# Optimization experiments

Hardware: AMD Instinct MI355X
Metric: run time of the kernel (lower is better)

## Reference

```python
import jax, jax.numpy as jnp
import numpy as np


def setup_inputs() -> dict:
    key = jax.random.key(0)
    k1, k2, k3, k4 = jax.random.split(key, 4)
    B, S, IN, H = 4, 2048, 512, 1024
    x = jax.random.normal(k1, (B, S, IN), dtype=jnp.float32)
    W1 = jax.random.normal(k2, (IN, H), dtype=jnp.float32) * (1.0 / np.sqrt(IN))
    b1 = jax.random.normal(k3, (H,), dtype=jnp.float32) * 0.02
    Wq = jax.random.normal(k4, (H, H), dtype=jnp.float32) * (1.0 / np.sqrt(H))
    return {"x": x, "W1": W1, "b1": b1, "Wq": Wq, "atten_size": 16}


def reference(x, W1, b1, Wq, atten_size):
    A = atten_size
    B, S, _ = x.shape
    H = W1.shape[1]
    h = jax.nn.relu(jnp.einsum('bsi,ih->bsh', x, W1) + b1)  # [B,S,H]
    # zero-pad sequence dim by A on each side
    padded = jnp.pad(h, ((0, 0), (A, A), (0, 0)))  # [B,S+2A,H]
    # torch: stack(roll(padded, k, 1) for k in -A..A, dim=2) then slice [A:-A]
    # => x_nei[b, i, j] = padded[b, 2A + i - j]
    idx = 2 * A + jnp.arange(S)[:, None] - jnp.arange(2 * A + 1)[None, :]  # [S,W]
    x_nei = padded[:, idx, :]  # [B,S,W,H]
    q = jnp.einsum('bsh,hk->bsk', h, Wq)  # [B,S,H]
    scores = jnp.einsum('bsh,bswh->bsw', q, x_nei) / jnp.sqrt(jnp.asarray(H, x.dtype))
    w = jax.nn.softmax(scores, axis=2)  # softmax over window axis
    out = jnp.einsum('bsw,bswh->bsh', w, x_nei)
    return out
```

## Files before the change

kernel.cpp:

```cpp
#include <hip/hip_runtime.h>
#include <stdint.h>

constexpr int BATCH = 4;
constexpr int SEQ   = 2048;
constexpr int DIN   = 512;
constexpr int DH    = 1024;
constexpr int BS    = BATCH * SEQ;
constexpr int AP    = 32;
constexpr int AW    = 64;

typedef float  floatx4 __attribute__((ext_vector_type(4)));
typedef short  bf16x8  __attribute__((ext_vector_type(8)));

static __device__ __forceinline__ unsigned short f2bf(float f) {
  union { float f; unsigned u; } v; v.f = f;
  unsigned r = (v.u + 0x7fffu + ((v.u >> 16) & 1u)) >> 16;
  return (unsigned short)r;
}

static __device__ __forceinline__ void gld_lds16(const unsigned short* g, const short* l) {
  typedef const __attribute__((address_space(1))) void* gvp;
  typedef __attribute__((address_space(3))) void* lvp;
  __builtin_amdgcn_global_load_lds((gvp)(uintptr_t)g, (lvp)(unsigned)(uintptr_t)l, 16, 0, 0);
}

__global__ __launch_bounds__(256) void prep_k(const float* __restrict__ X,
                                              const float* __restrict__ W1,
                                              const float* __restrict__ Wq,
                                              unsigned short* __restrict__ Xb,
                                              unsigned short* __restrict__ w1t,
                                              unsigned short* __restrict__ wqt) {
  __shared__ float t[32][33];
  if (blockIdx.y >= 48) {
    const int t0 = ((blockIdx.y - 48) * 32 + blockIdx.x) * 256 + threadIdx.x;
    const float4 a = ((const float4*)X)[(size_t)t0 * 2];
    const float4 b = ((const float4*)X)[(size_t)t0 * 2 + 1];
    __align__(16) unsigned short o[8];
    o[0] = f2bf(a.x); o[1] = f2bf(a.y); o[2] = f2bf(a.z); o[3] = f2bf(a.w);
    o[4] = f2bf(b.x); o[5] = f2bf(b.y); o[6] = f2bf(b.z); o[7] = f2bf(b.w);
    *(uint4*)(Xb + (size_t)t0 * 8) = *(const uint4*)o;
    return;
  }
  const bool isW1 = blockIdx.y < 16;
  const float* in = isW1 ? W1 : Wq;
  unsigned short* out = isW1 ? w1t : wqt;
  const int R = isW1 ? DIN : DH;
  const int C = DH;
  const int r0 = (isW1 ? blockIdx.y : (blockIdx.y - 16)) * 32;
  const int c0 = blockIdx.x * 32;
  const int tx = threadIdx.x & 31, ty = threadIdx.x >> 5;
  for (int i = ty; i < 32; i += 8) t[i][tx] = in[(size_t)(r0 + i) * C + c0 + tx];
  __syncthreads();
  for (int i = ty; i < 32; i += 8) out[(size_t)(c0 + i) * R + r0 + tx] = f2bf(t[tx][i]);
}

__global__ __launch_bounds__(256) void gemm1_k(const unsigned short* __restrict__ Ab,
                                               const unsigned short* __restrict__ Bt,
                                               const float* __restrict__ bias,
                                               unsigned short* __restrict__ outB,
                                               unsigned short* __restrict__ outBT) {
  const int M = BS, N = DH, K = DIN;
  __shared__ __align__(16) short As0[128 * 32], As1[128 * 32];
  __shared__ __align__(16) short Bs0[128 * 32], Bs1[128 * 32];
  const int tid  = threadIdx.x;
  const int m0   = blockIdx.x * 128, n0 = blockIdx.y * 128;
  const int wv   = tid >> 6, lane = tid & 63;
  const int wm   = (wv >> 1) * 64, wn = (wv & 1) * 64;
  const int l16  = lane & 15, quad = lane >> 4;

  const int ra = lane >> 2, ca = (lane & 3) * 8;
  const unsigned short* gA = Ab + (size_t)(m0 + wv * 32 + ra) * K + ca;
  const unsigned short* gB = Bt + (size_t)(n0 + wv * 32 + ra) * K + ca;
  const short* lA0a = &As0[wv * 1024];
  const short* lA0b = &As0[wv * 1024 + 512];
  const short* lA1a = &As1[wv * 1024];
  const short* lA1b = &As1[wv * 1024 + 512];
  const short* lB0a = &Bs0[wv * 1024];
  const short* lB0b = &Bs0[wv * 1024 + 512];
  const short* lB1a = &Bs1[wv * 1024];
  const short* lB1b = &Bs1[wv * 1024 + 512];

  floatx4 acc[4][4];
  for (int i = 0; i < 4; i++)
    for (int j = 0; j < 4; j++) acc[i][j] = {0.f, 0.f, 0.f, 0.f};

  for (int ks = 0; ks < K / 64; ++ks) {
    __syncthreads();
    gld_lds16(gA, lA0a); gld_lds16(gA + 16 * K, lA0b);
    gld_lds16(gA + 32, lA1a); gld_lds16(gA + 16 * K + 32, lA1b);
    gld_lds16(gB, lB0a); gld_lds16(gB + 16 * K, lB0b);
    gld_lds16(gB + 32, lB1a); gld_lds16(gB + 16 * K + 32, lB1b);
    gA += 64; gB += 64;
    __syncthreads();
    bf16x8 af[4], bfr[4];
    for (int i = 0; i < 4; i++)
      af[i] = *(const bf16x8*)&As0[(wm + i * 16 + l16) * 32 + quad * 8];
    for (int j = 0; j < 4; j++)
      bfr[j] = *(const bf16x8*)&Bs0[(wn + j * 16 + l16) * 32 + quad * 8];
    for (int i = 0; i < 4; i++)
      for (int j = 0; j < 4; j++)
        acc[i][j] = __builtin_amdgcn_mfma_f32_16x16x32_bf16(af[i], bfr[j], acc[i][j], 0, 0, 0);
    for (int i = 0; i < 4; i++)
      af[i] = *(const bf16x8*)&As1[(wm + i * 16 + l16) * 32 + quad * 8];
    for (int j = 0; j < 4; j++)
      bfr[j] = *(const bf16x8*)&Bs1[(wn + j * 16 + l16) * 32 + quad * 8];
    for (int i = 0; i < 4; i++)
      for (int j = 0; j < 4; j++)
        acc[i][j] = __builtin_amdgcn_mfma_f32_16x16x32_bf16(af[i], bfr[j], acc[i][j], 0, 0, 0);
  }

  for (int j = 0; j < 4; j++) {
    const int col = n0 + wn + j * 16 + l16;
    const float bv = bias[col];
    for (int i = 0; i < 4; i++) {
      const int rowb = m0 + wm + i * 16 + quad * 4;
      float v[4];
      for (int r = 0; r < 4; r++) v[r] = fmaxf(acc[i][j][r] + bv, 0.f);
      for (int r = 0; r < 4; r++) outB[(size_t)(rowb + r) * N + col] = f2bf(v[r]);
      ushort4 o4; o4.x = f2bf(v[0]); o4.y = f2bf(v[1]); o4.z = f2bf(v[2]); o4.w = f2bf(v[3]);
      *(ushort4*)(outBT + (size_t)col * M + rowb) = o4;
    }
  }
}

__global__ __launch_bounds__(1024, 4) void attn_fused_k(const unsigned short* __restrict__ hb,
                                                        const unsigned short* __restrict__ hbT,
                                                        const unsigned short* __restrict__ wqt,
                                                        float* __restrict__ out) {
  __shared__ __align__(16) unsigned short Hq[32 * 1024];
  __shared__ float Sf[2][32 * 64];
  __shared__ __align__(16) short Ps[32 * 72];

  const int tid  = threadIdx.x;
  const int wave = tid >> 6, lane = tid & 63;
  const int l16  = lane & 15, quad = lane >> 4;
  const int p0   = blockIdx.x * AP;
  const int s0   = p0 & (SEQ - 1);

  for (int i = tid; i < 32 * 72 / 2; i += 1024) ((unsigned*)Ps)[i] = 0;

  {
    const int r  = tid >> 5;
    const int c0 = (tid & 31) * 32;
    const unsigned short* src = hb + (size_t)(p0 + r) * DH + c0;
    #pragma unroll
    for (int c = 0; c < 4; c++) {
      uint4 v = *(const uint4*)(src + c * 8);
      const int colu = (c0 + c * 8) ^ ((r & 15) << 3);
      *(uint4*)&Hq[r * 1024 + colu] = v;
    }
  }
  __syncthreads();

  floatx4 qa[2][4];
  {
    for (int i = 0; i < 2; i++)
      for (int j = 0; j < 4; j++) qa[i][j] = {0.f, 0.f, 0.f, 0.f};
    const int wcol = wave * 64;
    const unsigned short* gq = wqt + (size_t)(wcol + l16) * DH + quad * 8;
    #pragma unroll 2
    for (int it = 0; it < 32; ++it) {
      const int cb = it * 32 + quad * 8;
      const int sw = cb ^ (l16 << 3);
      bf16x8 a0 = *(const bf16x8*)&Hq[l16 * 1024 + sw];
      bf16x8 a1 = *(const bf16x8*)&Hq[(16 + l16) * 1024 + sw];
      #pragma unroll
      for (int j = 0; j < 4; j++) {
        bf16x8 b = *(const bf16x8*)(gq + (size_t)(j * 16) * DH + it * 32);
        qa[0][j] = __builtin_amdgcn_mfma_f32_16x16x32_bf16(a0, b, qa[0][j], 0, 0, 0);
        qa[1][j] = __builtin_amdgcn_mfma_f32_16x16x32_bf16(a1, b, qa[1][j], 0, 0, 0);
      }
    }
  }
  __syncthreads();

  {
    const int wcol = wave * 64;
    for (int i = 0; i < 2; i++)
      for (int j = 0; j < 4; j++)
        for (int r = 0; r < 4; r++) {
          const int row  = i * 16 + quad * 4 + r;
          const int colu = wcol + j * 16 + l16;
          Hq[row * 1024 + (colu ^ ((row & 15) << 3))] = f2bf(qa[i][j][r]);
        }
  }
  __syncthreads();

  {
    const int kh = wave & 1;
    const int nt = (wave >> 1) & 3;
    const int mt = wave >> 3;
    const int qrow = mt * 16 + l16;
    const int hrow = s0 - 16 + nt * 16 + l16;
    const bool hv = (hrow >= 0) && (hrow < SEQ);
    const unsigned short* hp = hb + (long long)(p0 - 16 + nt * 16 + l16) * DH + kh * 512 + quad * 8;

    floatx4 ac[4] = {{0,0,0,0},{0,0,0,0},{0,0,0,0},{0,0,0,0}};
    const bf16x8 hz = {0,0,0,0,0,0,0,0};
    __builtin_amdgcn_s_setprio(1);
    #pragma unroll
    for (int it = 0; it < 16; ++it) {
      const int cb = kh * 512 + it * 32 + quad * 8;
      bf16x8 qf = *(const bf16x8*)&Hq[qrow * 1024 + (cb ^ (l16 << 3))];
      bf16x8 ha = hz;
      if (hv) ha = *(const bf16x8*)(hp + it * 32);
      ac[it & 3] = __builtin_amdgcn_mfma_f32_16x16x32_bf16(qf, ha, ac[it & 3], 0, 0, 0);
    }
    __builtin_amdgcn_s_setprio(0);
    floatx4 s4;
    for (int r = 0; r < 4; r++)
      s4[r] = (ac[0][r] + ac[1][r]) + (ac[2][r] + ac[3][r]);
    for (int r = 0; r < 4; r++)
      Sf[kh][(mt * 16 + quad * 4 + r) * 64 + nt * 16 + l16] = s4[r] * (1.f / 32.f);
  }
  __syncthreads();

  if (tid < 512) {
    const int row = tid >> 4, k = tid & 15;
    const float v0 = Sf[0][row * 64 + row + k] + Sf[1][row * 64 + row + k];
    const float v1 = Sf[0][row * 64 + row + k + 16] + Sf[1][row * 64 + row + k + 16];
    const float v2 = (k == 0) ? (Sf[0][row * 64 + row + 32] + Sf[1][row * 64 + row + 32]) : -1e30f;
    float mx = fmaxf(v0, fmaxf(v1, v2));
    for (int off = 1; off < 16; off <<= 1) mx = fmaxf(mx, __shfl_xor(mx, off, 64));
    const float e0 = __expf(v0 - mx), e1 = __expf(v1 - mx);
    const float e2 = (k == 0) ? __expf(v2 - mx) : 0.f;
    float sum = e0 + e1 + e2;
    for (int off = 1; off < 16; off <<= 1) sum += __shfl_xor(sum, off, 64);
    const float inv = 1.f / sum;
    Ps[row * 72 + row + k] = f2bf(e0 * inv);
    Ps[row * 72 + row + k + 16] = f2bf(e1 * inv);
    if (k == 0) Ps[row * 72 + row + 32] = f2bf(e2 * inv);
  }
  __syncthreads();

  {
    const bf16x8 pb00 = *(const bf16x8*)&Ps[(l16) * 72 + quad * 8];
    const bf16x8 pb01 = *(const bf16x8*)&Ps[(l16) * 72 + 32 + quad * 8];
    const bf16x8 pb10 = *(const bf16x8*)&Ps[(16 + l16) * 72 + quad * 8];
    const bf16x8 pb11 = *(const bf16x8*)&Ps[(16 + l16) * 72 + 32 + quad * 8];

    int lo = 16 - s0; if (lo < 0) lo = 0;
    int hi = SEQ + 16 - s0; if (hi > AW) hi = AW;
    const bool interior = (lo == 0) && (hi == AW);

    #pragma unroll
    for (int i = 0; i < 4; ++i) {
      const int mt2 = wave * 4 + i;
      const unsigned short* ap = hbT + (size_t)(mt2 * 16 + l16) * BS + (p0 - 16) + quad * 8;
      bf16x8 aa0 = *(const bf16x8*)(ap);
      bf16x8 aa1 = *(const bf16x8*)(ap + 32);
      if (!interior) {
        #pragma unroll
        for (int j = 0; j < 8; j++) {
          const int k = quad * 8 + j;
          if (k < lo || k >= hi) aa0[j] = 0;
          if (k + 32 < lo || k + 32 >= hi) aa1[j] = 0;
        }
      }
      floatx4 o0 = {0.f, 0.f, 0.f, 0.f}, o1 = {0.f, 0.f, 0.f, 0.f};
      __builtin_amdgcn_s_setprio(1);
      o0 = __builtin_amdgcn_mfma_f32_16x16x32_bf16(aa0, pb00, o0, 0, 0, 0);
      o0 = __builtin_amdgcn_mfma_f32_16x16x32_bf16(aa1, pb01, o0, 0, 0, 0);
      o1 = __builtin_amdgcn_mfma_f32_16x16x32_bf16(aa0, pb10, o1, 0, 0, 0);
      o1 = __builtin_amdgcn_mfma_f32_16x16x32_bf16(aa1, pb11, o1, 0, 0, 0);
      __builtin_amdgcn_s_setprio(0);
      float4 s0v; s0v.x = o0[0]; s0v.y = o0[1]; s0v.z = o0[2]; s0v.w = o0[3];
      float4 s1v; s1v.x = o1[0]; s1v.y = o1[1]; s1v.z = o1[2]; s1v.w = o1[3];
      *(float4*)(out + (size_t)(p0 + l16) * DH + mt2 * 16 + quad * 4) = s0v;
      *(float4*)(out + (size_t)(p0 + 16 + l16) * DH + mt2 * 16 + quad * 4) = s1v;
    }
  }
}

extern "C" void kernel_launch(void* const* d_in, const int* in_sizes, int n_in,
                              void* d_out, int out_size, void* d_ws, size_t ws_size,
                              hipStream_t stream) {
  const float* x  = (const float*)d_in[0];
  const float* W1 = (const float*)d_in[1];
  const float* b1 = (const float*)d_in[2];
  const float* Wq = (const float*)d_in[3];

  char* w = (char*)d_ws;
  unsigned short* w1t = (unsigned short*)(w);
  unsigned short* wqt = (unsigned short*)(w + (1ull  << 20));
  unsigned short* hb  = (unsigned short*)(w + (3ull  << 20));
  unsigned short* hbT = (unsigned short*)(w + (19ull << 20));
  unsigned short* xb  = (unsigned short*)(w + (35ull << 20));

  prep_k<<<dim3(32, 112), 256, 0, stream>>>(x, W1, Wq, xb, w1t, wqt);

  gemm1_k<<<dim3(BS / 128, DH / 128), 256, 0, stream>>>(xb, w1t, b1, hb, hbT);

  attn_fused_k<<<BS / AP, 1024, 0, stream>>>(hb, hbT, wqt, (float*)d_out);
}
```

Measured before the change: 186.6 us.

## Split Q projection into separate pipelined GEMM and read Q from global in attention

Moves the per-block Q = h·Wq projection out of the fused attention kernel into a second launch of a generalized GEMM kernel that writes Q to the workspace. The attention kernel then reads Q rows directly from global memory instead of staging h in LDS and recomputing. The GEMM is restructured with double-buffered A staging via LDS, B fragments loaded straight into registers, a swizzled block order, and setprio around MFMAs. This trades an extra kernel launch and a global round-trip for Q against the poor reuse of Wq in the old fused kernel, where each 32-row block reread all of Wq.

New measurement: 187.3 us. No clear change (+0.4%).

```diff
diff --git a/kernel.cpp b/kernel.cpp
--- a/kernel.cpp
+++ b/kernel.cpp
@@ -54,80 +54,104 @@
   for (int i = ty; i < 32; i += 8) out[(size_t)(c0 + i) * R + r0 + tx] = f2bf(t[tx][i]);
 }
 
-__global__ __launch_bounds__(256) void gemm1_k(const unsigned short* __restrict__ Ab,
-                                               const unsigned short* __restrict__ Bt,
-                                               const float* __restrict__ bias,
-                                               unsigned short* __restrict__ outB,
-                                               unsigned short* __restrict__ outBT) {
-  const int M = BS, N = DH, K = DIN;
-  __shared__ __align__(16) short As0[128 * 32], As1[128 * 32];
-  __shared__ __align__(16) short Bs0[128 * 32], Bs1[128 * 32];
-  const int tid  = threadIdx.x;
-  const int m0   = blockIdx.x * 128, n0 = blockIdx.y * 128;
-  const int wv   = tid >> 6, lane = tid & 63;
-  const int wm   = (wv >> 1) * 64, wn = (wv & 1) * 64;
-  const int l16  = lane & 15, quad = lane >> 4;
-
-  const int ra = lane >> 2, ca = (lane & 3) * 8;
-  const unsigned short* gA = Ab + (size_t)(m0 + wv * 32 + ra) * K + ca;
-  const unsigned short* gB = Bt + (size_t)(n0 + wv * 32 + ra) * K + ca;
-  const short* lA0a = &As0[wv * 1024];
-  const short* lA0b = &As0[wv * 1024 + 512];
-  const short* lA1a = &As1[wv * 1024];
-  const short* lA1b = &As1[wv * 1024 + 512];
-  const short* lB0a = &Bs0[wv * 1024];
-  const short* lB0b = &Bs0[wv * 1024 + 512];
-  const short* lB1a = &Bs1[wv * 1024];
-  const short* lB1b = &Bs1[wv * 1024 + 512];
+__global__ __launch_bounds__(256) void gemm_k(const unsigned short* __restrict__ Ab,
+                                              const unsigned short* __restrict__ Bt,
+                                              const float* __restrict__ bias,
+                                              unsigned short* __restrict__ outB,
+                                              unsigned short* __restrict__ outBT,
+                                              const int K) {
+  const int M = BS, N = DH;
+  __shared__ __align__(16) short As[2][2][128 * 32];
+  const int tid = threadIdx.x;
+  const int f   = blockIdx.x;
+  const int t   = (f & 7) * 64 + (f >> 3);
+  const int m0  = (t & 63) * 128, n0 = (t >> 6) * 128;
+  const int wv  = tid >> 6, lane = tid & 63;
+  const int wm  = (wv >> 1) * 64, wn = (wv & 1) * 64;
+  const int l16 = lane & 15, quad = lane >> 4;
+  const int ra  = lane >> 2, ca = (lane & 3) * 8;
+
+  const unsigned short* gA  = Ab + (size_t)(m0 + wv * 32 + ra) * K + ca;
+  const unsigned short* gB0 = Bt + (size_t)(n0 + wn + l16) * K + quad * 8;
 
   floatx4 acc[4][4];
   for (int i = 0; i < 4; i++)
     for (int j = 0; j < 4; j++) acc[i][j] = {0.f, 0.f, 0.f, 0.f};
 
-  for (int ks = 0; ks < K / 64; ++ks) {
+  bf16x8 b0[2][4], b1[2][4];
+
+  auto stageA = [&](int tb, int ks) {
+    const unsigned short* a = gA + ks * 64;
+    short* la = &As[tb][0][wv * 1024];
+    gld_lds16(a, la);
+    gld_lds16(a + 16 * K, la + 512);
+    short* lb = &As[tb][1][wv * 1024];
+    gld_lds16(a + 32, lb);
+    gld_lds16(a + 16 * K + 32, lb + 512);
+  };
+
+#define LOADB(dst, ks)                                                          \
+  _Pragma("unroll") for (int h = 0; h < 2; h++)                                 \
+  _Pragma("unroll") for (int j = 0; j < 4; j++)                                 \
+      dst[h][j] = *(const bf16x8*)(gB0 + (size_t)(j * 16) * K + (ks) * 64 + h * 32);
+
+#define COMPUTE(tb, bb)                                                         \
+  {                                                                             \
+    bf16x8 af[4];                                                               \
+    _Pragma("unroll") for (int h = 0; h < 2; h++) {                             \
+      _Pragma("unroll") for (int i = 0; i < 4; i++)                             \
+          af[i] = *(const bf16x8*)&As[tb][h][(wm + i * 16 + l16) * 32 + quad * 8]; \
+      __builtin_amdgcn_s_setprio(1);                                            \
+      _Pragma("unroll") for (int i = 0; i < 4; i++)                             \
+      _Pragma("unroll") for (int j = 0; j < 4; j++)                             \
+          acc[i][j] = __builtin_amdgcn_mfma_f32_16x16x32_bf16(af[i], bb[h][j],  \
+                                                              acc[i][j], 0, 0, 0); \
+      __builtin_amdgcn_s_setprio(0);                                            \
+    }                                                                           \
+  }
+
+  const int NK = K / 64;
+  LOADB(b0, 0);
+  stageA(0, 0);
+  __syncthreads();
+  for (int ks = 0; ks < NK; ks += 2) {
+    LOADB(b1, ks + 1);
+    stageA(1, ks + 1);
+    COMPUTE(0, b0);
     __syncthreads();
-    gld_lds16(gA, lA0a); gld_lds16(gA + 16 * K, lA0b);
-    gld_lds16(gA + 32, lA1a); gld_lds16(gA + 16 * K + 32, lA1b);
-    gld_lds16(gB, lB0a); gld_lds16(gB + 16 * K, lB0b);
-    gld_lds16(gB + 32, lB1a); gld_lds16(gB + 16 * K + 32, lB1b);
-    gA += 64; gB += 64;
+    if (ks + 2 < NK) {
+      LOADB(b0, ks + 2);
+      stageA(0, ks + 2);
+    }
+    COMPUTE(1, b1);
     __syncthreads();
-    bf16x8 af[4], bfr[4];
-    for (int i = 0; i < 4; i++)
-      af[i] = *(const bf16x8*)&As0[(wm + i * 16 + l16) * 32 + quad * 8];
-    for (int j = 0; j < 4; j++)
-      bfr[j] = *(const bf16x8*)&Bs0[(wn + j * 16 + l16) * 32 + quad * 8];
-    for (int i = 0; i < 4; i++)
-      for (int j = 0; j < 4; j++)
-        acc[i][j] = __builtin_amdgcn_mfma_f32_16x16x32_bf16(af[i], bfr[j], acc[i][j], 0, 0, 0);
-    for (int i = 0; i < 4; i++)
-      af[i] = *(const bf16x8*)&As1[(wm + i * 16 + l16) * 32 + quad * 8];
-    for (int j = 0; j < 4; j++)
-      bfr[j] = *(const bf16x8*)&Bs1[(wn + j * 16 + l16) * 32 + quad * 8];
-    for (int i = 0; i < 4; i++)
-      for (int j = 0; j < 4; j++)
-        acc[i][j] = __builtin_amdgcn_mfma_f32_16x16x32_bf16(af[i], bfr[j], acc[i][j], 0, 0, 0);
-  }
+  }
+#undef LOADB
+#undef COMPUTE
 
   for (int j = 0; j < 4; j++) {
     const int col = n0 + wn + j * 16 + l16;
-    const float bv = bias[col];
+    const float bv = bias ? bias[col] : 0.f;
     for (int i = 0; i < 4; i++) {
       const int rowb = m0 + wm + i * 16 + quad * 4;
       float v[4];
-      for (int r = 0; r < 4; r++) v[r] = fmaxf(acc[i][j][r] + bv, 0.f);
+      for (int r = 0; r < 4; r++) {
+        float x = acc[i][j][r] + bv;
+        v[r] = bias ? fmaxf(x, 0.f) : x;
+      }
       for (int r = 0; r < 4; r++) outB[(size_t)(rowb + r) * N + col] = f2bf(v[r]);
-      ushort4 o4; o4.x = f2bf(v[0]); o4.y = f2bf(v[1]); o4.z = f2bf(v[2]); o4.w = f2bf(v[3]);
-      *(ushort4*)(outBT + (size_t)col * M + rowb) = o4;
-    }
-  }
-}
-
-__global__ __launch_bounds__(1024, 4) void attn_fused_k(const unsigned short* __restrict__ hb,
-                                                        const unsigned short* __restrict__ hbT,
-                                                        const unsigned short* __restrict__ wqt,
-                                                        float* __restrict__ out) {
-  __shared__ __align__(16) unsigned short Hq[32 * 1024];
+      if (outBT) {
+        ushort4 o4; o4.x = f2bf(v[0]); o4.y = f2bf(v[1]); o4.z = f2bf(v[2]); o4.w = f2bf(v[3]);
+        *(ushort4*)(outBT + (size_t)col * M + rowb) = o4;
+      }
+    }
+  }
+}
+
+__global__ __launch_bounds__(1024) void attn_mfma_k(const unsigned short* __restrict__ hb,
+                                                    const unsigned short* __restrict__ hbT,
+                                                    const unsigned short* __restrict__ qb,
+                                                    float* __restrict__ out) {
   __shared__ float Sf[2][32 * 64];
   __shared__ __align__(16) short Ps[32 * 72];
 
@@ -140,57 +164,10 @@
   for (int i = tid; i < 32 * 72 / 2; i += 1024) ((unsigned*)Ps)[i] = 0;
 
   {
-    const int r  = tid >> 5;
-    const int c0 = (tid & 31) * 32;
-    const unsigned short* src = hb + (size_t)(p0 + r) * DH + c0;
-    #pragma unroll
-    for (int c = 0; c < 4; c++) {
-      uint4 v = *(const uint4*)(src + c * 8);
-      const int colu = (c0 + c * 8) ^ ((r & 15) << 3);
-      *(uint4*)&Hq[r * 1024 + colu] = v;
-    }
-  }
-  __syncthreads();
-
-  floatx4 qa[2][4];
-  {
-    for (int i = 0; i < 2; i++)
-      for (int j = 0; j < 4; j++) qa[i][j] = {0.f, 0.f, 0.f, 0.f};
-    const int wcol = wave * 64;
-    const unsigned short* gq = wqt + (size_t)(wcol + l16) * DH + quad * 8;
-    #pragma unroll 2
-    for (int it = 0; it < 32; ++it) {
-      const int cb = it * 32 + quad * 8;
-      const int sw = cb ^ (l16 << 3);
-      bf16x8 a0 = *(const bf16x8*)&Hq[l16 * 1024 + sw];
-      bf16x8 a1 = *(const bf16x8*)&Hq[(16 + l16) * 1024 + sw];
-      #pragma unroll
-      for (int j = 0; j < 4; j++) {
-        bf16x8 b = *(const bf16x8*)(gq + (size_t)(j * 16) * DH + it * 32);
-        qa[0][j] = __builtin_amdgcn_mfma_f32_16x16x32_bf16(a0, b, qa[0][j], 0, 0, 0);
-        qa[1][j] = __builtin_amdgcn_mfma_f32_16x16x32_bf16(a1, b, qa[1][j], 0, 0, 0);
-      }
-    }
-  }
-  __syncthreads();
-
-  {
-    const int wcol = wave * 64;
-    for (int i = 0; i < 2; i++)
-      for (int j = 0; j < 4; j++)
-        for (int r = 0; r < 4; r++) {
-          const int row  = i * 16 + quad * 4 + r;
-          const int colu = wcol + j * 16 + l16;
-          Hq[row * 1024 + (colu ^ ((row & 15) << 3))] = f2bf(qa[i][j][r]);
-        }
-  }
-  __syncthreads();
-
-  {
     const int kh = wave & 1;
     const int nt = (wave >> 1) & 3;
     const int mt = wave >> 3;
-    const int qrow = mt * 16 + l16;
+    const unsigned short* qp = qb + (size_t)(p0 + mt * 16 + l16) * DH + kh * 512 + quad * 8;
     const int hrow = s0 - 16 + nt * 16 + l16;
     const bool hv = (hrow >= 0) && (hrow < SEQ);
     const unsigned short* hp = hb + (long long)(p0 - 16 + nt * 16 + l16) * DH + kh * 512 + quad * 8;
@@ -200,11 +177,10 @@
     __builtin_amdgcn_s_setprio(1);
     #pragma unroll
     for (int it = 0; it < 16; ++it) {
-      const int cb = kh * 512 + it * 32 + quad * 8;
-      bf16x8 qf = *(const bf16x8*)&Hq[qrow * 1024 + (cb ^ (l16 << 3))];
+      bf16x8 qa = *(const bf16x8*)(qp + it * 32);
       bf16x8 ha = hz;
       if (hv) ha = *(const bf16x8*)(hp + it * 32);
-      ac[it & 3] = __builtin_amdgcn_mfma_f32_16x16x32_bf16(qf, ha, ac[it & 3], 0, 0, 0);
+      ac[it & 3] = __builtin_amdgcn_mfma_f32_16x16x32_bf16(qa, ha, ac[it & 3], 0, 0, 0);
     }
     __builtin_amdgcn_s_setprio(0);
     floatx4 s4;
@@ -285,11 +261,13 @@
   unsigned short* wqt = (unsigned short*)(w + (1ull  << 20));
   unsigned short* hb  = (unsigned short*)(w + (3ull  << 20));
   unsigned short* hbT = (unsigned short*)(w + (19ull << 20));
-  unsigned short* xb  = (unsigned short*)(w + (35ull << 20));
+  unsigned short* qb  = (unsigned short*)(w + (35ull << 20));
+  unsigned short* xb  = qb;
 
   prep_k<<<dim3(32, 112), 256, 0, stream>>>(x, W1, Wq, xb, w1t, wqt);
 
-  gemm1_k<<<dim3(BS / 128, DH / 128), 256, 0, stream>>>(xb, w1t, b1, hb, hbT);
-
-  attn_fused_k<<<BS / AP, 1024, 0, stream>>>(hb, hbT, wqt, (float*)d_out);
-}
+  gemm_k<<<512, 256, 0, stream>>>(xb, w1t, b1, hb, hbT, DIN);
+  gemm_k<<<512, 256, 0, stream>>>(hb, wqt, nullptr, qb, nullptr, DH);
+
+  attn_mfma_k<<<BS / AP, 1024, 0, stream>>>(hb, hbT, qb, (float*)d_out);
+}
```
